# Performance work log

Hardware: AMD Instinct MI355X
Metric: run time of the kernel (lower is better)

The kernel has to match this reference:

```python
import jax, jax.numpy as jnp
import numpy as np

N_HEAD = 16
POSE = 5
YAW = 1
END_X, END_Y = 18, 32
THETA = 1000.0
LN_EPS = 1e-5

def compute_axial_cis(dim, end_x, end_y, theta):
    # Axial 2D rotary: dim is per-head dim; dim//4 freqs per spatial axis.
    n = dim // 4
    freqs = 1.0 / (theta ** (jnp.arange(0, dim, 4)[:n].astype(jnp.float32) / dim))
    t = jnp.arange(end_x * end_y, dtype=jnp.float32)
    t_x = t % end_x
    t_y = jnp.floor(t / end_x)
    ang = jnp.concatenate([t_x[:, None] * freqs[None, :], t_y[:, None] * freqs[None, :]], axis=-1)  # [L, dim//2]
    return jnp.cos(ang), jnp.sin(ang)

def apply_rotary(x, cos, sin):
    # x: [B,H,L,D]; complex pairing = consecutive (even, odd) lanes, as in view_as_complex
    xe, xo = x[..., 0::2], x[..., 1::2]
    oe = xe * cos - xo * sin
    oo = xe * sin + xo * cos
    return jnp.stack([oe, oo], axis=-1).reshape(x.shape)

def layernorm(z, g, b):
    m = jnp.mean(z, axis=-1, keepdims=True)
    v = jnp.mean(jnp.square(z - m), axis=-1, keepdims=True)
    return (z - m) * jax.lax.rsqrt(v + LN_EPS) * g + b

def setup_inputs() -> dict:
    key = jax.random.key(0)
    ks = jax.random.split(key, 8)
    B, T, C = 16, 582, 1024
    x = jax.random.normal(ks[0], (B, T, C), dtype=jnp.float32)
    # additive causal mask (0 keep / -1e9 masked), as a float attn_mask
    causal = jnp.tril(jnp.ones((T, T), dtype=jnp.float32))
    attn_mask = jnp.broadcast_to(jnp.where(causal > 0, 0.0, -1e9), (B, T, T))
    s = 0.02
    Wq = jax.random.normal(ks[1], (C, C), dtype=jnp.float32) * s
    Wk = jax.random.normal(ks[2], (C, C), dtype=jnp.float32) * s
    Wv = jax.random.normal(ks[3], (C, C), dtype=jnp.float32) * s
    Wo = jax.random.normal(ks[4], (C, C), dtype=jnp.float32) * s
    q_ln_g = jnp.ones((C,), jnp.float32); q_ln_b = jnp.zeros((C,), jnp.float32)
    k_ln_g = jnp.ones((C,), jnp.float32); k_ln_b = jnp.zeros((C,), jnp.float32)
    return {"x": x, "attn_mask": attn_mask, "Wq": Wq, "Wk": Wk, "Wv": Wv, "Wo": Wo,
            "q_ln_g": q_ln_g, "q_ln_b": q_ln_b, "k_ln_g": k_ln_g, "k_ln_b": k_ln_b}

def reference(x, attn_mask, Wq, Wk, Wv, Wo, q_ln_g, q_ln_b, k_ln_g, k_ln_b):
    B, T, C = x.shape
    H = N_HEAD
    D = C // H
    q = layernorm(x @ Wq.T, q_ln_g, q_ln_b)
    k = layernorm(x @ Wk.T, k_ln_g, k_ln_b)
    v = (x @ Wv.T).reshape(B, T, H, D).transpose(0, 2, 1, 3)
    q = q.reshape(B, T, H, D).transpose(0, 2, 1, 3)
    k = k.reshape(B, T, H, D).transpose(0, 2, 1, 3)
    prefix = POSE + YAW
    if T > prefix:  # static shape condition
        cos, sin = compute_axial_cis(D, END_X, END_Y, THETA)
        L = T - prefix
        cos, sin = cos[:L], sin[:L]  # [L, D//2]
        q = jnp.concatenate([q[:, :, :prefix], apply_rotary(q[:, :, prefix:], cos, sin)], axis=2)
        k = jnp.concatenate([k[:, :, :prefix], apply_rotary(k[:, :, prefix:], cos, sin)], axis=2)
    scale = 1.0 / jnp.sqrt(jnp.float32(D))
    scores = jnp.einsum("bhqd,bhkd->bhqk", q, k) * scale + attn_mask[:, None, :, :]
    att = jax.nn.softmax(scores, axis=-1)
    y = jnp.einsum("bhqk,bhkd->bhqd", att, v)
    y = y.transpose(0, 2, 1, 3).reshape(B, T, C)
    return y @ Wo.T
```

## Files before the change

### kernel.cpp

```cpp
#include <hip/hip_runtime.h>
#include <hip/hip_bf16.h>

typedef short bf16x8 __attribute__((ext_vector_type(8)));
typedef short bf16x4 __attribute__((ext_vector_type(4)));
typedef float f32x4  __attribute__((ext_vector_type(4)));

#define LDP 72

__device__ __forceinline__ float bits2f(short u) {
  return __uint_as_float(((unsigned int)(unsigned short)u) << 16);
}
__device__ __forceinline__ short f2bits(float f) {
  __hip_bfloat16 h = __float2bfloat16(f);
  return *reinterpret_cast<short*>(&h);
}
__device__ __forceinline__ void gld16(const short* g, short* l) {
  __builtin_amdgcn_global_load_lds(
      (const __attribute__((address_space(1))) void*)g,
      (__attribute__((address_space(3))) void*)l, 16, 0, 0);
}

__global__ __launch_bounds__(256)
void cvt_x_kernel(const float* __restrict__ src, short* __restrict__ dst, long n) {
  long i = ((long)blockIdx.x * 256 + threadIdx.x) * 4;
  if (i + 3 < n) {
    float4 v = *(const float4*)(src + i);
    bf16x4 o;
    o[0] = f2bits(v.x); o[1] = f2bits(v.y); o[2] = f2bits(v.z); o[3] = f2bits(v.w);
    *(bf16x4*)(dst + i) = o;
  }
}

__global__ __launch_bounds__(256)
void cvt_w_kernel(const float* __restrict__ w0, const float* __restrict__ w1,
                  const float* __restrict__ w2, const float* __restrict__ w3,
                  short* __restrict__ dst) {
  long i = ((long)blockIdx.x * 256 + threadIdx.x) * 4;
  int sel = (int)(i >> 20);
  const float* s = (sel == 0) ? w0 : (sel == 1) ? w1 : (sel == 2) ? w2 : w3;
  long off = i & ((1L << 20) - 1);
  float4 v = *(const float4*)(s + off);
  bf16x4 o;
  o[0] = f2bits(v.x); o[1] = f2bits(v.y); o[2] = f2bits(v.z); o[3] = f2bits(v.w);
  *(bf16x4*)(dst + i) = o;
}

template<int MODE>
__global__ __launch_bounds__(256)
void gemm_nt(const short* __restrict__ A, const short* __restrict__ Bm,
             float* __restrict__ OutF, short* __restrict__ Oq,
             short* __restrict__ Ok, short* __restrict__ Ov,
             int M, int K, int N, int T, int TPAD) {
  __shared__ short As[128 * 64];
  __shared__ short Bs[128 * 64];
  const int tid = threadIdx.x;
  const int w = tid >> 6, l = tid & 63;
  const int wr = w >> 1, wc = w & 1;
  const int lg = l >> 4, lo = l & 15;
  const long row0 = (long)blockIdx.x * 128;
  const long col0 = (long)blockIdx.y * 128;

  const short* pa[4]; const short* pb[4]; short* la[4]; short* lb[4];
#pragma unroll
  for (int j = 0; j < 4; ++j) {
    const int ch = w * 4 + j;
    const int off = ch * 1024 + l * 16;
    const int row = off >> 7;
    const int lc  = (off & 127) ^ ((row & 7) << 4);
    long ga = row0 + row; if (ga > M - 1) ga = M - 1;
    pa[j] = &A[ga * K + (lc >> 1)];
    pb[j] = &Bm[(col0 + row) * K + (lc >> 1)];
    la[j] = &As[ch * 512];
    lb[j] = &Bs[ch * 512];
  }

  f32x4 acc[4][4] = {};

  for (int kt = 0; kt < K; kt += 64) {
    __syncthreads();
#pragma unroll
    for (int j = 0; j < 4; ++j) {
      gld16(pa[j] + kt, la[j]);
      gld16(pb[j] + kt, lb[j]);
    }
    __syncthreads();
    bf16x8 af[4][2], bfr[4][2];
#pragma unroll
    for (int mi = 0; mi < 4; ++mi)
#pragma unroll
      for (int ks = 0; ks < 2; ++ks) {
        int pe = (ks * 32 + lg * 8) ^ ((lo & 7) << 3);
        af[mi][ks] = *(const bf16x8*)(&As[(wr * 64 + mi * 16 + lo) * 64 + pe]);
      }
#pragma unroll
    for (int ni = 0; ni < 4; ++ni)
#pragma unroll
      for (int ks = 0; ks < 2; ++ks) {
        int pe = (ks * 32 + lg * 8) ^ ((lo & 7) << 3);
        bfr[ni][ks] = *(const bf16x8*)(&Bs[(wc * 64 + ni * 16 + lo) * 64 + pe]);
      }
#pragma unroll
    for (int mi = 0; mi < 4; ++mi)
#pragma unroll
      for (int ni = 0; ni < 4; ++ni)
#pragma unroll
        for (int ks = 0; ks < 2; ++ks)
          acc[mi][ni] = __builtin_amdgcn_mfma_f32_16x16x32_bf16(af[mi][ks], bfr[ni][ks], acc[mi][ni], 0, 0, 0);
  }

#pragma unroll
  for (int mi = 0; mi < 4; ++mi) {
#pragma unroll
    for (int r = 0; r < 4; ++r) {
      long m = row0 + wr * 64 + mi * 16 + lg * 4 + r;
      if (m >= M) continue;
#pragma unroll
      for (int ni = 0; ni < 4; ++ni) {
        long n = col0 + wc * 64 + ni * 16 + lo;
        float v = acc[mi][ni][r];
        if constexpr (MODE == 2) {
          OutF[m * (long)N + n] = v;
        } else {
          if (n < 1024) {
            Oq[m * 1024 + n] = f2bits(v);
          } else if (n < 2048) {
            Ok[m * 1024 + (n - 1024)] = f2bits(v);
          } else {
            long b = m / T, t = m - b * T;
            long nn = n - 2048, h = nn >> 6, dd = nn & 63;
            Ov[((b * 16 + h) * 64 + dd) * TPAD + t] = f2bits(v);
          }
        }
      }
    }
  }
}

__global__ __launch_bounds__(256)
void ln_rope_kernel(const short* __restrict__ qpre, const short* __restrict__ kpre,
                    const float* __restrict__ qg, const float* __restrict__ qb2,
                    const float* __restrict__ kg, const float* __restrict__ kb2,
                    short* __restrict__ qa, short* __restrict__ ka, int T) {
  const int row = blockIdx.x;
  const short* in; const float *g, *be; short* out;
  if (blockIdx.y == 0) { in = qpre; g = qg; be = qb2; out = qa; }
  else                 { in = kpre; g = kg; be = kb2; out = ka; }
  const int tid = threadIdx.x;
  const int c0 = tid * 4;

  bf16x4 xv = *(const bf16x4*)(&in[(long)row * 1024 + c0]);
  float xf[4];
  float s = 0.f, sq = 0.f;
#pragma unroll
  for (int i = 0; i < 4; ++i) { xf[i] = bits2f(xv[i]); s += xf[i]; sq += xf[i] * xf[i]; }
#pragma unroll
  for (int o = 1; o < 64; o <<= 1) { s += __shfl_xor(s, o); sq += __shfl_xor(sq, o); }
  __shared__ float red[8];
  const int w = tid >> 6, l = tid & 63;
  if (l == 0) { red[w] = s; red[4 + w] = sq; }
  __syncthreads();
  s  = red[0] + red[1] + red[2] + red[3];
  sq = red[4] + red[5] + red[6] + red[7];
  const float mean = s * (1.0f / 1024.0f);
  const float var  = sq * (1.0f / 1024.0f) - mean * mean;
  const float rstd = rsqrtf(var + 1e-5f);

  float4 gv = *(const float4*)(&g[c0]);
  float4 bv = *(const float4*)(&be[c0]);
  float z[4];
  z[0] = (xf[0] - mean) * rstd * gv.x + bv.x;
  z[1] = (xf[1] - mean) * rstd * gv.y + bv.y;
  z[2] = (xf[2] - mean) * rstd * gv.z + bv.z;
  z[3] = (xf[3] - mean) * rstd * gv.w + bv.w;

  const int t = row % T;
  const int p = t - 6;
  if (p >= 0) {
    const float tx = (float)(p % 18);
    const float ty = (float)(p / 18);
    const int jbase = (c0 & 63) >> 1;
#pragma unroll
    for (int q2 = 0; q2 < 2; ++q2) {
      const int jj = jbase + q2;
      const int i  = jj & 15;
      const float freq = exp2f(-(float)i * 0.6228615177913804f);
      const float ang  = ((jj < 16) ? tx : ty) * freq;
      float sv, cv;
      sincosf(ang, &sv, &cv);
      const float xe = z[q2 * 2], xo = z[q2 * 2 + 1];
      z[q2 * 2]     = xe * cv - xo * sv;
      z[q2 * 2 + 1] = xe * sv + xo * cv;
    }
  }
  const long b = row / T;
  const int h = c0 >> 6, d = c0 & 63;
  bf16x4 ov;
#pragma unroll
  for (int i = 0; i < 4; ++i) ov[i] = f2bits(z[i]);
  *(bf16x4*)(&out[(((b * 16 + h) * T) + t) * 64 + d]) = ov;
}

__global__ __launch_bounds__(256)
void attn_kernel(const short* __restrict__ Q, const short* __restrict__ Kk,
                 const short* __restrict__ Vt, short* __restrict__ Y,
                 int T, int TPAD) {
  __shared__ short Ks[2][64 * 64];
  __shared__ short Vs[2][64 * 64];
  __shared__ short Ps[4][16 * LDP];
  const int tid = threadIdx.x;
  const int w = tid >> 6, l = tid & 63, lg = l >> 4, lo = l & 15;
  const int qb = gridDim.x - 1 - blockIdx.x;
  const int bh = blockIdx.y;
  const int b = bh >> 4, h = bh & 15;
  const long qbase = (long)bh * T * 64;
  const long vbase = (long)bh * 64;
  short* Pw = &Ps[w][0];

  int srow[2], scolb[2];
#pragma unroll
  for (int p = 0; p < 2; ++p) {
    int off = p * 4096 + tid * 16;
    srow[p] = off >> 7;
    scolb[p] = (off & 127) ^ ((srow[p] & 7) << 4);
  }
  auto STAGE = [&](int kt, int buf) {
#pragma unroll
    for (int p = 0; p < 2; ++p) {
      short* kd = &Ks[buf][(p * 4096 + w * 1024) >> 1];
      short* vd = &Vs[buf][(p * 4096 + w * 1024) >> 1];
      gld16(&Kk[qbase + (long)(kt * 64 + srow[p]) * 64 + (scolb[p] >> 1)], kd);
      gld16(&Vt[(vbase + srow[p]) * TPAD + (long)kt * 64 + (scolb[p] >> 1)], vd);
    }
  };

  const long qrow_l = qb * 64 + w * 16 + lo;
  bf16x8 qf[2];
  qf[0] = *(const bf16x8*)(&Q[qbase + qrow_l * 64 + lg * 8]);
  qf[1] = *(const bf16x8*)(&Q[qbase + qrow_l * 64 + 32 + lg * 8]);

  float mrow[4], lsum[4];
  f32x4 oacc[4] = {};
#pragma unroll
  for (int r = 0; r < 4; ++r) { mrow[r] = -3e38f; lsum[r] = 0.f; }
  const float SCL = 0.125f * 1.44269504f;
  const int nkt = qb + 1;

  STAGE(0, 0);
  for (int kt = 0; kt < nkt; ++kt) {
    const int cur = kt & 1;
    __syncthreads();
    if (kt + 1 < nkt) STAGE(kt + 1, cur ^ 1);

    f32x4 sf[4] = {};
    __builtin_amdgcn_s_setprio(1);
#pragma unroll
    for (int ni = 0; ni < 4; ++ni)
#pragma unroll
      for (int kk = 0; kk < 2; ++kk) {
        int pe = (kk * 32 + lg * 8) ^ ((lo & 7) << 3);
        bf16x8 kfr = *(const bf16x8*)(&Ks[cur][(ni * 16 + lo) * 64 + pe]);
        sf[ni] = __builtin_amdgcn_mfma_f32_16x16x32_bf16(qf[kk], kfr, sf[ni], 0, 0, 0);
      }
    __builtin_amdgcn_s_setprio(0);

    float pm[4][4], tmax[4];
#pragma unroll
    for (int r = 0; r < 4; ++r) tmax[r] = -3e38f;
#pragma unroll
    for (int ni = 0; ni < 4; ++ni)
#pragma unroll
      for (int r = 0; r < 4; ++r) {
        int key  = kt * 64 + ni * 16 + lo;
        int qrow = qb * 64 + w * 16 + lg * 4 + r;
        float sv = sf[ni][r] * SCL;
        if (key > qrow || key >= T) sv = -3e38f;
        pm[ni][r] = sv;
        tmax[r] = fmaxf(tmax[r], sv);
      }
#pragma unroll
    for (int r = 0; r < 4; ++r)
#pragma unroll
      for (int o = 1; o < 16; o <<= 1) tmax[r] = fmaxf(tmax[r], __shfl_xor(tmax[r], o));

    bool need = !__all(tmax[0] <= mrow[0] && tmax[1] <= mrow[1] &&
                       tmax[2] <= mrow[2] && tmax[3] <= mrow[3]);
    if (need) {
#pragma unroll
      for (int r = 0; r < 4; ++r) {
        float mn = fmaxf(mrow[r], tmax[r]);
        float fsc = exp2f(mrow[r] - mn);
        mrow[r] = mn;
        lsum[r] *= fsc;
#pragma unroll
        for (int ni = 0; ni < 4; ++ni) oacc[ni][r] *= fsc;
      }
    }
    float psum[4] = {0.f, 0.f, 0.f, 0.f};
#pragma unroll
    for (int ni = 0; ni < 4; ++ni)
#pragma unroll
      for (int r = 0; r < 4; ++r) {
        float pv = exp2f(pm[ni][r] - mrow[r]);
        pm[ni][r] = pv;
        psum[r] += pv;
      }
#pragma unroll
    for (int r = 0; r < 4; ++r) {
#pragma unroll
      for (int o = 1; o < 16; o <<= 1) psum[r] += __shfl_xor(psum[r], o);
      lsum[r] += psum[r];
    }

#pragma unroll
    for (int ni = 0; ni < 4; ++ni)
#pragma unroll
      for (int r = 0; r < 4; ++r)
        Pw[(lg * 4 + r) * LDP + ni * 16 + lo] = f2bits(pm[ni][r]);

    __builtin_amdgcn_s_setprio(1);
#pragma unroll
    for (int kk = 0; kk < 2; ++kk) {
      bf16x8 pf = *(const bf16x8*)(&Pw[lo * LDP + kk * 32 + lg * 8]);
#pragma unroll
      for (int ni = 0; ni < 4; ++ni) {
        int pe = (kk * 32 + lg * 8) ^ ((lo & 7) << 3);
        bf16x8 vf = *(const bf16x8*)(&Vs[cur][(ni * 16 + lo) * 64 + pe]);
        oacc[ni] = __builtin_amdgcn_mfma_f32_16x16x32_bf16(pf, vf, oacc[ni], 0, 0, 0);
      }
    }
    __builtin_amdgcn_s_setprio(0);
  }

#pragma unroll
  for (int r = 0; r < 4; ++r) {
    int tq = qb * 64 + w * 16 + lg * 4 + r;
    if (tq >= T) continue;
    float inv = 1.0f / lsum[r];
#pragma unroll
    for (int ni = 0; ni < 4; ++ni) {
      float o = oacc[ni][r] * inv;
      Y[((long)b * T + tq) * 1024 + h * 64 + ni * 16 + lo] = f2bits(o);
    }
  }
}

extern "C" void kernel_launch(void* const* d_in, const int* in_sizes, int n_in,
                              void* d_out, int out_size, void* d_ws, size_t ws_size,
                              hipStream_t stream) {
  const float* x   = (const float*)d_in[0];
  const float* Wq  = (const float*)d_in[2];
  const float* Wk  = (const float*)d_in[3];
  const float* Wv  = (const float*)d_in[4];
  const float* Wo  = (const float*)d_in[5];
  const float* qg  = (const float*)d_in[6];
  const float* qb2 = (const float*)d_in[7];
  const float* kg  = (const float*)d_in[8];
  const float* kb2 = (const float*)d_in[9];

  const int B = 16, T = 582, C = 1024;
  const int M = B * T;
  const int TPAD = 584;

  short* ws = (short*)d_ws;
  const long E  = (long)M * C;
  const long EV = (long)B * 16 * 64 * TPAD;
  short* xb   = ws;
  short* qpre = ws + E;
  short* kpre = ws + 2 * E;
  short* ka   = ws + 3 * E;
  short* vat  = ws + 4 * E;
  short* wb   = ws + 4 * E + EV + 1024;
  short* qa   = xb;
  short* y    = qpre;
  float* out  = (float*)d_out;
  (void)ws_size; (void)in_sizes; (void)n_in; (void)out_size;

  const long WE = 1L << 20;

  cvt_x_kernel<<<(int)(E / 4 / 256), 256, 0, stream>>>(x, xb, E);
  cvt_w_kernel<<<(int)(4 * WE / 4 / 256), 256, 0, stream>>>(Wq, Wk, Wv, Wo, wb);

  dim3 gqkv((M + 127) / 128, 3072 / 128);
  gemm_nt<3><<<gqkv, 256, 0, stream>>>(xb, wb, nullptr, qpre, kpre, vat, M, C, 3072, T, TPAD);
  ln_rope_kernel<<<dim3(M, 2), 256, 0, stream>>>(qpre, kpre, qg, qb2, kg, kb2, qa, ka, T);
  attn_kernel<<<dim3((T + 63) / 64, B * 16), 256, 0, stream>>>(qa, ka, vat, y, T, TPAD);
  dim3 gout((M + 127) / 128, C / 128);
  gemm_nt<2><<<gout, 256, 0, stream>>>(y, wb + 3 * WE, out, nullptr, nullptr, nullptr, M, C, C, T, TPAD);
}
```

Baseline: 264.6 us.

## Replace QKV GEMM with 256x256 8-wave double-buffered pipelined kernel

The fused QKV projection GEMM moves to a dedicated kernel with 256x256 tiles, 512 threads and double-buffered LDS. It interleaves global-to-LDS loads with MFMA phases using explicit vmcnt waits, barriers and setprio, and remaps workgroup IDs so that contiguous tiles share an XCD. The goal is to hide memory latency and raise MFMA utilisation and L2 reuse on the largest GEMM. The trade-offs are higher LDS and register use (one workgroup per CU), fewer workgroups (about 37x12) for M=9312, and hand-tuned synchronisation that is fragile.

New measurement: 329.8 us. 24.7% more time.

```diff
diff --git a/kernel.cpp b/kernel.cpp
--- a/kernel.cpp
+++ b/kernel.cpp
@@ -6,6 +6,9 @@
 typedef float f32x4  __attribute__((ext_vector_type(4)));
 
 #define LDP 72
+
+#define S_VMCNT(N) asm volatile("s_waitcnt vmcnt(" #N ")" ::: "memory")
+#define S_BAR()    do { asm volatile("" ::: "memory"); __builtin_amdgcn_s_barrier(); asm volatile("" ::: "memory"); } while (0)
 
 __device__ __forceinline__ float bits2f(short u) {
   return __uint_as_float(((unsigned int)(unsigned short)u) << 16);
@@ -45,12 +48,136 @@
   *(bf16x4*)(dst + i) = o;
 }
 
-template<int MODE>
+__global__ __launch_bounds__(512, 1)
+void gemm_qkv_8p(const short* __restrict__ A, const short* __restrict__ Bm,
+                 short* __restrict__ Oq, short* __restrict__ Ok, short* __restrict__ Ov,
+                 int M, int T, int TPAD) {
+  const int K = 1024, NT = 16;
+  __shared__ short As[2][16384];
+  __shared__ short Bs[2][16384];
+  const int tid = threadIdx.x;
+  const int w = tid >> 6, l = tid & 63;
+  const int wm = w >> 2, wn = w & 3;
+  const int lg = l >> 4, lo = l & 15;
+
+  const int gx = gridDim.x;
+  const int nwg = gx * gridDim.y;
+  const int flat = blockIdx.y * gx + blockIdx.x;
+  const int q8 = nwg >> 3, r8 = nwg & 7;
+  const int xcd = flat & 7, idx = flat >> 3;
+  const int wgid = (xcd < r8 ? xcd * (q8 + 1) : r8 * (q8 + 1) + (xcd - r8) * q8) + idx;
+  const long row0 = (long)(wgid % gx) * 256;
+  const long col0 = (long)(wgid / gx) * 256;
+
+  const int srow = tid >> 3;
+  const int scb  = ((tid * 16) & 127) ^ ((srow & 7) << 4);
+  const short* pA[4];
+#pragma unroll
+  for (int q = 0; q < 4; ++q) {
+    long ra = row0 + q * 64 + srow; if (ra > M - 1) ra = M - 1;
+    pA[q] = &A[ra * K + (scb >> 1)];
+  }
+  const short* pBe[2]; const short* pBo[2];
+#pragma unroll
+  for (int p = 0; p < 2; ++p) {
+    int rho = p * 64 + srow;
+    pBe[p] = &Bm[(col0 + (rho >> 5) * 64 + (rho & 31)) * K + (scb >> 1)];
+    pBo[p] = &Bm[(col0 + (rho >> 5) * 64 + 32 + (rho & 31)) * K + (scb >> 1)];
+  }
+
+#define STG_AQ(T2, Q) gld16(pA[Q] + (T2) * 64, &As[(T2) & 1][(Q) * 4096 + w * 512])
+#define STG_BE(T2) do { gld16(pBe[0] + (T2) * 64, &Bs[(T2) & 1][w * 512]); \
+                        gld16(pBe[1] + (T2) * 64, &Bs[(T2) & 1][4096 + w * 512]); } while (0)
+#define STG_BO(T2) do { gld16(pBo[0] + (T2) * 64, &Bs[(T2) & 1][8192 + w * 512]); \
+                        gld16(pBo[1] + (T2) * 64, &Bs[(T2) & 1][12288 + w * 512]); } while (0)
+
+  bf16x8 af[4][2], bfr[2][2];
+  f32x4 acc[8][4] = {};
+
+#define LDA8(S, MH) \
+  _Pragma("unroll") for (int m = 0; m < 4; ++m) \
+    _Pragma("unroll") for (int ks = 0; ks < 2; ++ks) \
+      af[m][ks] = *(const bf16x8*)(&As[S][(wm * 128 + ((MH) * 4 + m) * 16 + lo) * 64 + ((ks * 32 + lg * 8) ^ ((lo & 7) << 3))]);
+#define LDB4(S, NH) \
+  _Pragma("unroll") for (int n = 0; n < 2; ++n) \
+    _Pragma("unroll") for (int ks = 0; ks < 2; ++ks) \
+      bfr[n][ks] = *(const bf16x8*)(&Bs[S][((NH) * 128 + wn * 32 + n * 16 + lo) * 64 + ((ks * 32 + lg * 8) ^ ((lo & 7) << 3))]);
+#define MFMA16(MH, NH) do { \
+    asm volatile("s_waitcnt lgkmcnt(0)" ::: "memory"); \
+    __builtin_amdgcn_sched_barrier(0); \
+    __builtin_amdgcn_s_setprio(1); \
+    _Pragma("unroll") for (int ks = 0; ks < 2; ++ks) \
+      _Pragma("unroll") for (int m = 0; m < 4; ++m) \
+        _Pragma("unroll") for (int n = 0; n < 2; ++n) \
+          acc[(MH) * 4 + m][(NH) * 2 + n] = __builtin_amdgcn_mfma_f32_16x16x32_bf16( \
+              af[m][ks], bfr[n][ks], acc[(MH) * 4 + m][(NH) * 2 + n], 0, 0, 0); \
+    __builtin_amdgcn_s_setprio(0); \
+  } while (0)
+
+  STG_AQ(0, 0); STG_AQ(0, 2);
+  STG_BO(0);
+  STG_AQ(0, 1); STG_AQ(0, 3);
+  STG_BE(0);
+  STG_AQ(1, 0); STG_AQ(1, 2);
+  STG_BO(1);
+  STG_AQ(1, 1); STG_AQ(1, 3);
+  S_VMCNT(6);
+  S_BAR();
+
+  for (int t = 0; t < NT; ++t) {
+    const int s = t & 1;
+    LDA8(s, 0); LDB4(s, 0);
+    if (t + 1 < NT) STG_BE(t + 1);
+    MFMA16(0, 0);
+    S_BAR();
+    LDB4(s, 1);
+    if (t + 2 < NT) { STG_AQ(t + 2, 0); STG_AQ(t + 2, 2); }
+    MFMA16(0, 1);
+    S_BAR();
+    LDA8(s, 1);
+    if (t + 2 < NT) STG_BO(t + 2);
+    MFMA16(1, 1);
+    S_BAR();
+    LDB4(s, 0);
+    if (t + 2 < NT) { STG_AQ(t + 2, 1); STG_AQ(t + 2, 3); }
+    MFMA16(1, 0);
+    if (t < NT - 2) { S_VMCNT(6); } else if (t == NT - 2) { S_VMCNT(0); }
+    S_BAR();
+  }
+#undef STG_AQ
+#undef STG_BE
+#undef STG_BO
+#undef LDA8
+#undef LDB4
+#undef MFMA16
+
+#pragma unroll
+  for (int m = 0; m < 8; ++m) {
+#pragma unroll
+    for (int r = 0; r < 4; ++r) {
+      long gm = row0 + wm * 128 + m * 16 + lg * 4 + r;
+      if (gm >= M) continue;
+#pragma unroll
+      for (int p = 0; p < 4; ++p) {
+        long n = col0 + wn * 64 + p * 16 + lo;
+        float v = acc[m][p][r];
+        if (n < 1024) {
+          Oq[gm * 1024 + n] = f2bits(v);
+        } else if (n < 2048) {
+          Ok[gm * 1024 + (n - 1024)] = f2bits(v);
+        } else {
+          long b = gm / T, t2 = gm - b * T;
+          long nn = n - 2048, h = nn >> 6, d = nn & 63;
+          Ov[((b * 16 + h) * 64 + d) * TPAD + t2] = f2bits(v);
+        }
+      }
+    }
+  }
+}
+
 __global__ __launch_bounds__(256)
-void gemm_nt(const short* __restrict__ A, const short* __restrict__ Bm,
-             float* __restrict__ OutF, short* __restrict__ Oq,
-             short* __restrict__ Ok, short* __restrict__ Ov,
-             int M, int K, int N, int T, int TPAD) {
+void gemm_out(const short* __restrict__ A, const short* __restrict__ Bm,
+              float* __restrict__ OutF, int M, int K, int N) {
   __shared__ short As[128 * 64];
   __shared__ short Bs[128 * 64];
   const int tid = threadIdx.x;
@@ -117,20 +244,7 @@
 #pragma unroll
       for (int ni = 0; ni < 4; ++ni) {
         long n = col0 + wc * 64 + ni * 16 + lo;
-        float v = acc[mi][ni][r];
-        if constexpr (MODE == 2) {
-          OutF[m * (long)N + n] = v;
-        } else {
-          if (n < 1024) {
-            Oq[m * 1024 + n] = f2bits(v);
-          } else if (n < 2048) {
-            Ok[m * 1024 + (n - 1024)] = f2bits(v);
-          } else {
-            long b = m / T, t = m - b * T;
-            long nn = n - 2048, h = nn >> 6, dd = nn & 63;
-            Ov[((b * 16 + h) * 64 + dd) * TPAD + t] = f2bits(v);
-          }
-        }
+        OutF[m * (long)N + n] = acc[mi][ni][r];
       }
     }
   }
@@ -380,10 +494,10 @@
   cvt_x_kernel<<<(int)(E / 4 / 256), 256, 0, stream>>>(x, xb, E);
   cvt_w_kernel<<<(int)(4 * WE / 4 / 256), 256, 0, stream>>>(Wq, Wk, Wv, Wo, wb);
 
-  dim3 gqkv((M + 127) / 128, 3072 / 128);
-  gemm_nt<3><<<gqkv, 256, 0, stream>>>(xb, wb, nullptr, qpre, kpre, vat, M, C, 3072, T, TPAD);
+  dim3 gqkv((M + 255) / 256, 3072 / 256);
+  gemm_qkv_8p<<<gqkv, 512, 0, stream>>>(xb, wb, qpre, kpre, vat, M, T, TPAD);
   ln_rope_kernel<<<dim3(M, 2), 256, 0, stream>>>(qpre, kpre, qg, qb2, kg, kb2, qa, ka, T);
   attn_kernel<<<dim3((T + 63) / 64, B * 16), 256, 0, stream>>>(qa, ka, vat, y, T, TPAD);
   dim3 gout((M + 127) / 128, C / 128);
-  gemm_nt<2><<<gout, 256, 0, stream>>>(y, wb + 3 * WE, out, nullptr, nullptr, nullptr, M, C, C, T, TPAD);
-}
+  gemm_out<<<gout, 256, 0, stream>>>(y, wb + 3 * WE, out, M, C, C);
+}
```
